# Kernel tuning notes

Hardware: AMD Instinct MI355X
Metric: run time of the kernel (lower is better)

The kernel has to match this reference:

```python
import jax, jax.numpy as jnp
import numpy as np

B, CH, H, W = 4, 256, 48, 160
A = 36            # num anchors
STRIDE = 8
KH = KW = 3       # kernel size
K2 = KH * KW
PAD = 1
THRESH = 0.5
TOPK = 3


def _offset_table():
    """Replicates shape_align.__init__ offset buffer: [1, A, 2*K2, H, W].
    Channel 2*k is the h-offset, 2*k+1 the w-offset for kernel tap k=i*KW+j."""
    rng = np.random.default_rng(0)
    ws = rng.uniform(16.0, 400.0, A).astype(np.float32)   # anchor widths (px)
    hs = rng.uniform(16.0, 300.0, A).astype(np.float32)   # anchor heights (px)
    hstep = hs / STRIDE / KH
    wstep = ws / STRIDE / KW
    off = np.zeros((1, A, 2 * K2, H, W), np.float32)
    for i in range(KH):
        for j in range(KW):
            kk = i * KW + j
            off[0, :, 2 * kk, :, :] = ((hstep - 1.0) * (i - KH / 2 + 0.5))[:, None, None]
            off[0, :, 2 * kk + 1, :, :] = ((wstep - 1.0) * (j - KW / 2 + 0.5))[:, None, None]
    return jnp.asarray(off)


def setup_inputs() -> dict:
    key = jax.random.key(0)
    k1, k2, k3 = jax.random.split(key, 3)
    x = jax.random.normal(k1, (B, CH, H, W), jnp.float32)
    prob = jax.random.uniform(k2, (B, A, H, W), jnp.float32)  # in [0,1), thresh=0.5
    weight = jax.random.normal(k3, (CH, CH, KH, KW), jnp.float32) * 0.02
    bias = jnp.zeros((CH,), jnp.float32)
    return {"x": x, "prob": prob, "offset_table": _offset_table(),
            "weight": weight, "bias": bias, "k": TOPK}


def _dcnv2(x, offset, mask, weight, bias):
    """Modulated deformable conv v2, stride=1, pad=1, dilation=1, 1 deform group.
    x: [B,C,H,W]; offset: [B,2*K2,H,W] ((h,w) interleaved); mask: [B,K2,H,W]."""
    b, c, h, w = x.shape
    off = offset.reshape(b, K2, 2, h, w)
    ki = (jnp.arange(K2) // KW - PAD).astype(x.dtype)   # kernel row offsets
    kj = (jnp.arange(K2) % KW - PAD).astype(x.dtype)    # kernel col offsets
    hg = jnp.arange(h, dtype=x.dtype)
    wg = jnp.arange(w, dtype=x.dtype)
    py = hg[None, None, :, None] + ki[None, :, None, None] + off[:, :, 0]  # [B,K2,H,W]
    px = wg[None, None, None, :] + kj[None, :, None, None] + off[:, :, 1]
    y0 = jnp.floor(py); x0 = jnp.floor(px)
    dy = py - y0; dx = px - x0
    y0i = y0.astype(jnp.int32); x0i = x0.astype(jnp.int32)
    y1i = y0i + 1;              x1i = x0i + 1
    xflat = x.reshape(b, c, h * w)

    def corner(yi, xi, wgt):
        valid = ((yi >= 0) & (yi < h) & (xi >= 0) & (xi < w)).astype(x.dtype)
        idx = (jnp.clip(yi, 0, h - 1) * w + jnp.clip(xi, 0, w - 1)).reshape(b, 1, K2 * h * w)
        g = jnp.take_along_axis(xflat, idx, axis=2)          # [B,C,K2*H*W]
        return g * (wgt * valid).reshape(b, 1, K2 * h * w)

    val = (corner(y0i, x0i, (1 - dy) * (1 - dx)) +
           corner(y0i, x1i, (1 - dy) * dx) +
           corner(y1i, x0i, dy * (1 - dx)) +
           corner(y1i, x1i, dy * dx))
    col = val.reshape(b, c, K2, h, w) * mask[:, None]        # modulation
    out = jnp.einsum('ock,bckhw->bohw', weight.reshape(weight.shape[0], c, K2), col)
    return out + bias[None, :, None, None]


def _forward(x, prob, offset_table, weight, bias, k):
    b, _, h, w = x.shape
    noff = offset_table.shape[2]                              # 2*K2
    # top-k anchor gating over anchor axis
    pk, ik = jax.lax.top_k(jnp.transpose(prob, (0, 2, 3, 1)), k)  # [B,H,W,k]
    pk = jnp.transpose(pk, (0, 3, 1, 2))                      # [B,k,H,W]
    ik = jnp.transpose(ik, (0, 3, 1, 2))
    sm = jax.nn.softmax(pk, axis=1)
    m = jnp.max(pk, axis=1, keepdims=True)                    # [B,1,H,W]
    hard = (m > THRESH).astype(x.dtype)
    # gather per-pixel offsets of the selected anchors
    tab = jnp.broadcast_to(offset_table, (b,) + offset_table.shape[1:])
    idx = jnp.broadcast_to(ik[:, :, None], (b, k, noff, h, w))
    off = jnp.take_along_axis(tab, idx, axis=1)               # [B,k,2*K2,H,W]
    off = jnp.sum(off * sm[:, :, None], axis=1) * hard        # [B,2*K2,H,W]
    mrep = jnp.repeat(m, K2, axis=1)                          # [B,K2,H,W]
    return _dcnv2(x, off, mrep, weight, bias) + x


def reference(x, prob, offset_table, weight, bias, k):
    return _forward(x, prob, offset_table, weight, bias, k)
```

## Files before the change

### kernel.cpp

```cpp
#include <hip/hip_runtime.h>
#include <math.h>

#define B_    4
#define CH_   256
#define H_    48
#define W_    160
#define A_    36
#define K2_   9
#define HW_   (H_*W_)
#define NPIX_ (B_*HW_)
#define KTOT_ (CH_*K2_)
#define CPC_  32
#define KC_   (CPC_*K2_)
#define NCHK_ (CH_/CPC_)
#define NKST_ (KTOT_/32)
#define LSTR_ 296
#define PT2_  64
#define NBLK_ (NPIX_/PT2_)

typedef __attribute__((ext_vector_type(8))) short bf16x8;
typedef __attribute__((ext_vector_type(4))) float f32x4;

__device__ inline ushort f2bf(float f) {
    union { float f; unsigned u; } c; c.f = f;
    unsigned r = c.u + 0x7FFFu + ((c.u >> 16) & 1u);
    return (ushort)(r >> 16);
}
__device__ inline float bf2f(ushort u) {
    union { unsigned u; float f; } c; c.u = (unsigned)u << 16; return c.f;
}

__global__ __launch_bounds__(256)
void prep_weight2(const float* __restrict__ w, ushort* __restrict__ wp2) {
    int t = blockIdx.x * 256 + threadIdx.x;
    if (t >= CH_ * KTOT_) return;
    int j    = t & 7;
    int lane = (t >> 3) & 63;
    int kk   = t >> 9;
    int kst  = kk % NKST_;
    int rg   = kk / NKST_;
    int row  = rg * 16 + (lane & 15);
    int kq   = kst * 32 + (lane >> 4) * 8 + j;
    int chunk = kq / KC_, r = kq % KC_;
    int tap = r / CPC_, ci = r % CPC_;
    int c = chunk * CPC_ + ci;
    wp2[t] = f2bf(w[(row * CH_ + c) * K2_ + tap]);
}

__global__ __launch_bounds__(256)
void prep_weight(const float* __restrict__ w, ushort* __restrict__ wp) {
    int t = blockIdx.x * 256 + threadIdx.x;
    if (t >= CH_ * KTOT_) return;
    int o  = t / KTOT_, kk = t % KTOT_;
    int chunk = kk / KC_, r = kk % KC_;
    int tap = r / CPC_, ci = r % CPC_;
    int c = chunk * CPC_ + ci;
    wp[t] = f2bf(w[(o * CH_ + c) * K2_ + tap]);
}

__global__ __launch_bounds__(256)
void prep_xt(const float* __restrict__ x, ushort* __restrict__ xt) {
    int bid = blockIdx.x;
    int hwT = bid % (HW_ / 128);
    int rest = bid / (HW_ / 128);
    int cT = rest & 3;
    int b  = rest >> 2;
    int hw0 = hwT * 128, c0 = cT * 64;
    int tid = threadIdx.x;
    int u = tid & 7, s = tid >> 3;
    const float* xb = x + ((long)b * CH_ + c0 + u * 8) * HW_ + hw0 + s * 4;
    float4 L[8];
    #pragma unroll
    for (int i = 0; i < 8; ++i) L[i] = *(const float4*)(xb + (long)i * HW_);
    ushort* xo = xt + ((long)b * HW_ + hw0 + s * 4) * CH_ + c0 + u * 8;
    #pragma unroll
    for (int j = 0; j < 4; ++j) {
        bf16x8 o;
        #pragma unroll
        for (int i = 0; i < 8; ++i) {
            float f = (j == 0) ? L[i].x : (j == 1) ? L[i].y : (j == 2) ? L[i].z : L[i].w;
            o[i] = (short)f2bf(f);
        }
        *(bf16x8*)(xo + (long)j * CH_) = o;
    }
}

__global__ __launch_bounds__(256)
void gating_kernel(const float* __restrict__ prob,
                   const float* __restrict__ table,
                   float* __restrict__ m_out,
                   float* __restrict__ off_out) {
    int pix = blockIdx.x * 256 + threadIdx.x;
    if (pix >= NPIX_) return;
    int b  = pix / HW_;
    int hw = pix % HW_;
    const float* pr = prob + (long)b * A_ * HW_ + hw;

    float v0 = -1e30f, v1 = -1e30f, v2 = -1e30f;
    int   i0 = 0, i1 = 0, i2 = 0;
    #pragma unroll 4
    for (int a = 0; a < A_; ++a) {
        float v = pr[(long)a * HW_];
        if (v > v0)      { v2=v1; i2=i1; v1=v0; i1=i0; v0=v; i0=a; }
        else if (v > v1) { v2=v1; i2=i1; v1=v;  i1=a; }
        else if (v > v2) { v2=v;  i2=a; }
    }
    float e1 = expf(v1 - v0), e2 = expf(v2 - v0);
    float inv = 1.0f / (1.0f + e1 + e2);
    float s0 = inv, s1 = e1*inv, s2 = e2*inv;
    float hard = (v0 > 0.5f) ? 1.0f : 0.0f;

    m_out[pix] = v0;
    const float* t0 = table + ((long)i0 * 18) * HW_ + hw;
    const float* t1 = table + ((long)i1 * 18) * HW_ + hw;
    const float* t2 = table + ((long)i2 * 18) * HW_ + hw;
    float* op = off_out + (long)pix * 18;
    #pragma unroll
    for (int c = 0; c < 18; ++c) {
        float o = s0 * t0[(long)c * HW_] + s1 * t1[(long)c * HW_] + s2 * t2[(long)c * HW_];
        op[c] = o * hard;
    }
}

__global__ __launch_bounds__(576)
void conv_mfma11(const float* __restrict__ x,
                 const ushort* __restrict__ xt,
                 const ushort* __restrict__ wp2,
                 const float* __restrict__ prob,
                 const float* __restrict__ table,
                 const float* __restrict__ bias,
                 float* __restrict__ out) {
    __shared__ __align__(16) ushort col[2][PT2_ * LSTR_];
    __shared__ float off_l[PT2_ * 18];
    __shared__ float m_l[PT2_];

    const int tid  = threadIdx.x;
    const int lane = tid & 63;
    const int wv   = tid >> 6;
    const int l15  = lane & 15;
    const int l16  = lane >> 4;
    const int bid  = (int)blockIdx.x;
    const int bswz = (bid & 7) * (NBLK_ / 8) + (bid >> 3);
    const int pb   = bswz * PT2_;
    const int b    = pb / HW_;
    const int hw0  = pb % HW_;
    const long xb  = (long)b * CH_ * HW_;
    const ushort* xtb = xt + (long)b * HW_ * CH_;

    if (tid < PT2_) {
        const int px = tid;
        const int hw = hw0 + px;
        const float* pr = prob + (long)b * A_ * HW_ + hw;
        float v0 = -1e30f, v1 = -1e30f, v2 = -1e30f;
        int   i0 = 0, i1 = 0, i2 = 0;
        #pragma unroll 4
        for (int a = 0; a < A_; ++a) {
            float v = pr[(long)a * HW_];
            if (v > v0)      { v2=v1; i2=i1; v1=v0; i1=i0; v0=v; i0=a; }
            else if (v > v1) { v2=v1; i2=i1; v1=v;  i1=a; }
            else if (v > v2) { v2=v;  i2=a; }
        }
        float e1 = expf(v1 - v0), e2 = expf(v2 - v0);
        float inv = 1.0f / (1.0f + e1 + e2);
        float s0 = inv, s1 = e1*inv, s2 = e2*inv;
        float hard = (v0 > 0.5f) ? 1.0f : 0.0f;
        m_l[px] = v0;
        const float* t0 = table + ((long)i0 * 18) * HW_ + hw;
        const float* t1 = table + ((long)i1 * 18) * HW_ + hw;
        const float* t2 = table + ((long)i2 * 18) * HW_ + hw;
        #pragma unroll
        for (int c = 0; c < 18; ++c) {
            float o = s0 * t0[(long)c * HW_] + s1 * t1[(long)c * HW_] + s2 * t2[(long)c * HW_];
            off_l[px * 18 + c] = o * hard;
        }
    }
    __syncthreads();

    const int sseg = lane & 3;
    const int qd   = lane >> 2;
    int   coff[4][4];
    float cwgt[4][4];
    int   dsto[4];
    #pragma unroll
    for (int g = 0; g < 4; ++g) {
        int pr = g * 144 + wv * 16 + qd;
        int px = pr & 63, kt = pr >> 6;
        int hw = hw0 + px;
        int h  = hw / W_, w_ = hw % W_;
        float m    = m_l[px];
        float offh = off_l[px * 18 + 2*kt];
        float offw = off_l[px * 18 + 2*kt + 1];
        float py  = (float)(h  + (kt / 3 - 1)) + offh;
        float pxf = (float)(w_ + (kt % 3 - 1)) + offw;
        float y0f = floorf(py), x0f = floorf(pxf);
        float dy = py - y0f,   dx = pxf - x0f;
        int y0 = (int)y0f, x0i = (int)x0f;
        int y1 = y0 + 1,   x1  = x0i + 1;
        float vy0 = (y0  >= 0 && y0  < H_) ? 1.f : 0.f;
        float vy1 = (y1  >= 0 && y1  < H_) ? 1.f : 0.f;
        float vx0 = (x0i >= 0 && x0i < W_) ? 1.f : 0.f;
        float vx1 = (x1  >= 0 && x1  < W_) ? 1.f : 0.f;
        int cy0 = min(max(y0, 0),  H_-1), cy1 = min(max(y1, 0), H_-1);
        int cx0 = min(max(x0i, 0), W_-1), cx1 = min(max(x1, 0), W_-1);
        coff[g][0] = (cy0*W_ + cx0) * CH_;  cwgt[g][0] = (1.f-dy)*(1.f-dx)*vy0*vx0*m;
        coff[g][1] = (cy0*W_ + cx1) * CH_;  cwgt[g][1] = (1.f-dy)*dx      *vy0*vx1*m;
        coff[g][2] = (cy1*W_ + cx0) * CH_;  cwgt[g][2] = dy      *(1.f-dx)*vy1*vx0*m;
        coff[g][3] = (cy1*W_ + cx1) * CH_;  cwgt[g][3] = dy      *dx      *vy1*vx1*m;
        dsto[g] = px * LSTR_ + kt * CPC_ + sseg * 8;
    }

    f32x4 acc[2][4];
    #pragma unroll
    for (int m = 0; m < 2; ++m)
        #pragma unroll
        for (int n = 0; n < 4; ++n)
            acc[m][n] = (f32x4)(0.f);

    const int rg0 = wv * 2;
    const int mg  = wv * 32;

    bf16x8 d[2][4];

    auto LOADpair = [&](int chI, int g0) {
        const int cb0 = chI * CPC_ + sseg * 8;
        #pragma unroll
        for (int gg = 0; gg < 2; ++gg)
            #pragma unroll
            for (int c = 0; c < 4; ++c)
                d[gg][c] = *(const bf16x8*)(xtb + coff[g0 + gg][c] + cb0);
    };
    auto WRITEpair = [&](int bufi, int g0) {
        #pragma unroll
        for (int gg = 0; gg < 2; ++gg) {
            float a8[8];
            #pragma unroll
            for (int j = 0; j < 8; ++j) a8[j] = 0.f;
            #pragma unroll
            for (int c = 0; c < 4; ++c) {
                float wgt = cwgt[g0 + gg][c];
                #pragma unroll
                for (int j = 0; j < 8; ++j)
                    a8[j] = fmaf(wgt, bf2f((ushort)d[gg][c][j]), a8[j]);
            }
            bf16x8 o;
            #pragma unroll
            for (int j = 0; j < 8; ++j) o[j] = (short)f2bf(a8[j]);
            *(bf16x8*)(&col[bufi][dsto[g0 + gg]]) = o;
        }
    };
    auto COMPUTEhalf = [&](int bufi, int chI, int ks0, int ks1) {
        if (wv < 8) {
            for (int ks = ks0; ks < ks1; ++ks) {
                const int kst = chI * K2_ + ks;
                const ushort* wr = wp2 + (((long)rg0 * NKST_ + kst) << 9) + (lane << 3);
                bf16x8 a0 = *(const bf16x8*)(wr);
                bf16x8 a1 = *(const bf16x8*)(wr + (1l * NKST_ << 9));
                const ushort* cb = &col[bufi][l15 * LSTR_ + ks * 32 + 8 * l16];
                bf16x8 b0 = *(const bf16x8*)(cb);
                bf16x8 b1 = *(const bf16x8*)(cb + 16 * LSTR_);
                bf16x8 b2 = *(const bf16x8*)(cb + 32 * LSTR_);
                bf16x8 b3 = *(const bf16x8*)(cb + 48 * LSTR_);
                __builtin_amdgcn_s_setprio(1);
                acc[0][0] = __builtin_amdgcn_mfma_f32_16x16x32_bf16(a0, b0, acc[0][0], 0, 0, 0);
                acc[0][1] = __builtin_amdgcn_mfma_f32_16x16x32_bf16(a0, b1, acc[0][1], 0, 0, 0);
                acc[0][2] = __builtin_amdgcn_mfma_f32_16x16x32_bf16(a0, b2, acc[0][2], 0, 0, 0);
                acc[0][3] = __builtin_amdgcn_mfma_f32_16x16x32_bf16(a0, b3, acc[0][3], 0, 0, 0);
                acc[1][0] = __builtin_amdgcn_mfma_f32_16x16x32_bf16(a1, b0, acc[1][0], 0, 0, 0);
                acc[1][1] = __builtin_amdgcn_mfma_f32_16x16x32_bf16(a1, b1, acc[1][1], 0, 0, 0);
                acc[1][2] = __builtin_amdgcn_mfma_f32_16x16x32_bf16(a1, b2, acc[1][2], 0, 0, 0);
                acc[1][3] = __builtin_amdgcn_mfma_f32_16x16x32_bf16(a1, b3, acc[1][3], 0, 0, 0);
                __builtin_amdgcn_s_setprio(0);
            }
        }
    };

    LOADpair(0, 0); WRITEpair(0, 0);
    LOADpair(0, 2); WRITEpair(0, 2);
    __syncthreads();

    for (int chI = 0; chI < NCHK_; ++chI) {
        const int cur = chI & 1, nxt = cur ^ 1;
        const bool pf = (chI < NCHK_ - 1);
        if (pf) LOADpair(chI + 1, 0);
        COMPUTEhalf(cur, chI, 0, 4);
        if (pf) { WRITEpair(nxt, 0); LOADpair(chI + 1, 2); }
        COMPUTEhalf(cur, chI, 4, 9);
        if (pf) WRITEpair(nxt, 2);
        __syncthreads();
    }

    if (wv < 8) {
        #pragma unroll
        for (int m = 0; m < 2; ++m)
            #pragma unroll
            for (int n = 0; n < 4; ++n)
                #pragma unroll
                for (int r = 0; r < 4; ++r) {
                    int o  = mg + m * 16 + l16 * 4 + r;
                    int hw = hw0 + n * 16 + l15;
                    long oi = xb + (long)o * HW_ + hw;
                    out[oi] = acc[m][n][r] + bias[o] + x[oi];
                }
    }
}

__global__ __launch_bounds__(576)
void conv_mfma2(const float* __restrict__ x,
                const ushort* __restrict__ wp,
                const float* __restrict__ bias,
                const float* __restrict__ m_arr,
                const float* __restrict__ off_arr,
                float* __restrict__ out) {
    __shared__ __align__(16) ushort col[PT2_ * LSTR_];

    const int tid  = threadIdx.x;
    const int lane = tid & 63;
    const int wv   = tid >> 6;
    const int l15  = lane & 15;
    const int l16  = lane >> 4;
    const int pb   = blockIdx.x * PT2_;
    const int b    = pb / HW_;
    const int hw0  = pb % HW_;
    const long xb  = (long)b * CH_ * HW_;

    int   id0, id1, id2, id3;
    float wg0, wg1, wg2, wg3;
    {
        int px = lane, kt = wv;
        int hw = hw0 + px;
        int h  = hw / W_, w_ = hw % W_;
        int pix = b * HW_ + hw;
        float m    = m_arr[pix];
        float offh = off_arr[(long)pix * 18 + 2*kt];
        float offw = off_arr[(long)pix * 18 + 2*kt + 1];
        float py = (float)(h  + (kt / 3 - 1)) + offh;
        float px_= (float)(w_ + (kt % 3 - 1)) + offw;
        float y0f = floorf(py), x0f = floorf(px_);
        float dy = py - y0f,   dx = px_ - x0f;
        int y0 = (int)y0f, x0 = (int)x0f;
        int y1 = y0 + 1,   x1 = x0 + 1;
        float vy0 = (y0 >= 0 && y0 < H_) ? 1.f : 0.f;
        float vy1 = (y1 >= 0 && y1 < H_) ? 1.f : 0.f;
        float vx0 = (x0 >= 0 && x0 < W_) ? 1.f : 0.f;
        float vx1 = (x1 >= 0 && x1 < W_) ? 1.f : 0.f;
        int cy0 = min(max(y0, 0), H_-1), cy1 = min(max(y1, 0), H_-1);
        int cx0 = min(max(x0, 0), W_-1), cx1 = min(max(x1, 0), W_-1);
        id0 = cy0*W_ + cx0;  wg0 = (1.f-dy)*(1.f-dx)*vy0*vx0*m;
        id1 = cy0*W_ + cx1;  wg1 = (1.f-dy)*dx      *vy0*vx1*m;
        id2 = cy1*W_ + cx0;  wg2 = dy      *(1.f-dx)*vy1*vx0*m;
        id3 = cy1*W_ + cx1;  wg3 = dy      *dx      *vy1*vx1*m;
    }

    f32x4 acc[4][2];
    #pragma unroll
    for (int m = 0; m < 4; ++m)
        #pragma unroll
        for (int n = 0; n < 2; ++n)
            acc[m][n] = (f32x4)(0.f);

    const int mg = (wv & 3) * 64;
    const int pg = (wv >> 2) * 32;

    for (int chI = 0; chI < NCHK_; ++chI) {
        __syncthreads();
        {
            const int c0 = chI * CPC_;
            ushort* dst = &col[lane * LSTR_ + wv * CPC_];
            #pragma unroll
            for (int c8 = 0; c8 < 4; ++c8) {
                bf16x8 pk;
                #pragma unroll
                for (int j = 0; j < 8; ++j) {
                    const float* xs = x + xb + (long)(c0 + c8*8 + j) * HW_;
                    float v = wg0 * xs[id0] + wg1 * xs[id1]
                            + wg2 * xs[id2] + wg3 * xs[id3];
                    pk[j] = (short)f2bf(v);
                }
                *(bf16x8*)(dst + c8 * 8) = pk;
            }
        }
        __syncthreads();
        if (wv < 8) {
            #pragma unroll
            for (int ks = 0; ks < K2_; ++ks) {
                const int kg = chI * KC_ + ks * 32 + 8 * l16;
                const ushort* wr = wp + (long)(mg + l15) * KTOT_ + kg;
                bf16x8 a0 = *(const bf16x8*)(wr);
                bf16x8 a1 = *(const bf16x8*)(wr + 16 * KTOT_);
                bf16x8 a2 = *(const bf16x8*)(wr + 32 * KTOT_);
                bf16x8 a3 = *(const bf16x8*)(wr + 48 * KTOT_);
                const ushort* cb = &col[(pg + l15) * LSTR_ + ks * 32 + 8 * l16];
                bf16x8 b0 = *(const bf16x8*)(cb);
                bf16x8 b1 = *(const bf16x8*)(cb + 16 * LSTR_);
                acc[0][0] = __builtin_amdgcn_mfma_f32_16x16x32_bf16(a0, b0, acc[0][0], 0, 0, 0);
                acc[0][1] = __builtin_amdgcn_mfma_f32_16x16x32_bf16(a0, b1, acc[0][1], 0, 0, 0);
                acc[1][0] = __builtin_amdgcn_mfma_f32_16x16x32_bf16(a1, b0, acc[1][0], 0, 0, 0);
                acc[1][1] = __builtin_amdgcn_mfma_f32_16x16x32_bf16(a1, b1, acc[1][1], 0, 0, 0);
                acc[2][0] = __builtin_amdgcn_mfma_f32_16x16x32_bf16(a2, b0, acc[2][0], 0, 0, 0);
                acc[2][1] = __builtin_amdgcn_mfma_f32_16x16x32_bf16(a2, b1, acc[2][1], 0, 0, 0);
                acc[3][0] = __builtin_amdgcn_mfma_f32_16x16x32_bf16(a3, b0, acc[3][0], 0, 0, 0);
                acc[3][1] = __builtin_amdgcn_mfma_f32_16x16x32_bf16(a3, b1, acc[3][1], 0, 0, 0);
            }
        }
    }

    if (wv < 8) {
        #pragma unroll
        for (int m = 0; m < 4; ++m)
            #pragma unroll
            for (int n = 0; n < 2; ++n)
                #pragma unroll
                for (int r = 0; r < 4; ++r) {
                    int o  = mg + m * 16 + l16 * 4 + r;
                    int hw = hw0 + pg + n * 16 + l15;
                    long oi = xb + (long)o * HW_ + hw;
                    out[oi] = acc[m][n][r] + bias[o] + x[oi];
                }
    }
}

extern "C" void kernel_launch(void* const* d_in, const int* in_sizes, int n_in,
                              void* d_out, int out_size, void* d_ws, size_t ws_size,
                              hipStream_t stream) {
    const float* x      = (const float*)d_in[0];
    const float* prob   = (const float*)d_in[1];
    const float* table  = (const float*)d_in[2];
    const float* weight = (const float*)d_in[3];
    const float* bias   = (const float*)d_in[4];
    float* out = (float*)d_out;

    const size_t wp_bytes  = (size_t)CH_ * KTOT_ * 2;
    const size_t m_bytes   = (size_t)NPIX_ * 4;
    const size_t off_bytes = (size_t)NPIX_ * 18 * 4;
    const size_t xt_bytes  = (size_t)NPIX_ * CH_ * 2;

    ushort* wp_ws  = (ushort*)d_ws;
    float*  m_ws   = (float*)((char*)d_ws + wp_bytes);
    float*  off_ws = (float*)((char*)d_ws + wp_bytes + m_bytes);
    ushort* xt_ws  = (ushort*)((char*)d_ws + wp_bytes + m_bytes + off_bytes);

    if (ws_size >= wp_bytes + m_bytes + off_bytes + xt_bytes) {
        prep_weight2<<<(CH_ * KTOT_ + 255) / 256, 256, 0, stream>>>(weight, wp_ws);
        prep_xt<<<(HW_ / 128) * 4 * B_, 256, 0, stream>>>(x, xt_ws);
        conv_mfma11<<<NBLK_, 576, 0, stream>>>(x, xt_ws, wp_ws, prob, table, bias, out);
    } else {
        gating_kernel<<<NPIX_ / 256, 256, 0, stream>>>(prob, table, m_ws, off_ws);
        prep_weight<<<(CH_ * KTOT_ + 255) / 256, 256, 0, stream>>>(weight, wp_ws);
        conv_mfma2<<<NPIX_ / PT2_, 576, 0, stream>>>(x, wp_ws, bias, m_ws, off_ws, out);
    }
}
```

Measured before the change: 140.3 us.

## Split deformable conv into separate im2col kernel and LDS-streamed GEMM kernel

Adds an im2col kernel that computes gating and bilinear-sampled bf16 columns into a large global workspace, then a GEMM kernel that streams those columns into LDS with direct global-to-LDS loads and double buffering. The intent is to decouple the irregular gather from the MFMA loop so each kernel runs without the other's stalls. The cost is a large round trip of the column buffer through HBM, and the path only runs if the workspace is big enough.

```diff
diff --git a/kernel.cpp b/kernel.cpp
--- a/kernel.cpp
+++ b/kernel.cpp
@@ -17,6 +17,8 @@
 #define LSTR_ 296
 #define PT2_  64
 #define NBLK_ (NPIX_/PT2_)
+#define COLB_ 36864
+#define COLW_ (COLB_/2)
 
 typedef __attribute__((ext_vector_type(8))) short bf16x8;
 typedef __attribute__((ext_vector_type(4))) float f32x4;
@@ -28,6 +30,13 @@
 }
 __device__ inline float bf2f(ushort u) {
     union { unsigned u; float f; } c; c.u = (unsigned)u << 16; return c.f;
+}
+
+__device__ inline void gld_lds16(const ushort* g, ushort* l) {
+    __builtin_amdgcn_global_load_lds(
+        (const __attribute__((address_space(1))) unsigned int*)(g),
+        (__attribute__((address_space(3))) unsigned int*)(l),
+        16, 0, 0);
 }
 
 __global__ __launch_bounds__(256)
@@ -119,6 +128,206 @@
     for (int c = 0; c < 18; ++c) {
         float o = s0 * t0[(long)c * HW_] + s1 * t1[(long)c * HW_] + s2 * t2[(long)c * HW_];
         op[c] = o * hard;
+    }
+}
+
+__global__ __launch_bounds__(576)
+void im2col_k(const ushort* __restrict__ xt,
+              const float* __restrict__ prob,
+              const float* __restrict__ table,
+              ushort* __restrict__ colg) {
+    __shared__ float off_l[PT2_ * 18];
+    __shared__ float m_l[PT2_];
+
+    const int tid  = threadIdx.x;
+    const int lane = tid & 63;
+    const int wv   = tid >> 6;
+    const int bid  = (int)blockIdx.x;
+    const int bswz = (bid & 7) * (NBLK_ / 8) + (bid >> 3);
+    const int pb   = bswz * PT2_;
+    const int b    = pb / HW_;
+    const int hw0  = pb % HW_;
+    const ushort* xtb = xt + (long)b * HW_ * CH_;
+    ushort* cg = colg + (long)bswz * (NCHK_ * COLW_);
+
+    if (tid < PT2_) {
+        const int px = tid;
+        const int hw = hw0 + px;
+        const float* pr = prob + (long)b * A_ * HW_ + hw;
+        float v0 = -1e30f, v1 = -1e30f, v2 = -1e30f;
+        int   i0 = 0, i1 = 0, i2 = 0;
+        #pragma unroll 4
+        for (int a = 0; a < A_; ++a) {
+            float v = pr[(long)a * HW_];
+            if (v > v0)      { v2=v1; i2=i1; v1=v0; i1=i0; v0=v; i0=a; }
+            else if (v > v1) { v2=v1; i2=i1; v1=v;  i1=a; }
+            else if (v > v2) { v2=v;  i2=a; }
+        }
+        float e1 = expf(v1 - v0), e2 = expf(v2 - v0);
+        float inv = 1.0f / (1.0f + e1 + e2);
+        float s0 = inv, s1 = e1*inv, s2 = e2*inv;
+        float hard = (v0 > 0.5f) ? 1.0f : 0.0f;
+        m_l[px] = v0;
+        const float* t0 = table + ((long)i0 * 18) * HW_ + hw;
+        const float* t1 = table + ((long)i1 * 18) * HW_ + hw;
+        const float* t2 = table + ((long)i2 * 18) * HW_ + hw;
+        #pragma unroll
+        for (int c = 0; c < 18; ++c) {
+            float o = s0 * t0[(long)c * HW_] + s1 * t1[(long)c * HW_] + s2 * t2[(long)c * HW_];
+            off_l[px * 18 + c] = o * hard;
+        }
+    }
+    __syncthreads();
+
+    const int sseg = lane & 3;
+    const int qd   = lane >> 2;
+    int   coff[4][4];
+    float cwgt[4][4];
+    int   gdst[4];
+    #pragma unroll
+    for (int g = 0; g < 4; ++g) {
+        int pr = g * 144 + wv * 16 + qd;
+        int px = pr & 63, kt = pr >> 6;
+        int hw = hw0 + px;
+        int h  = hw / W_, w_ = hw % W_;
+        float m    = m_l[px];
+        float offh = off_l[px * 18 + 2*kt];
+        float offw = off_l[px * 18 + 2*kt + 1];
+        float py  = (float)(h  + (kt / 3 - 1)) + offh;
+        float pxf = (float)(w_ + (kt % 3 - 1)) + offw;
+        float y0f = floorf(py), x0f = floorf(pxf);
+        float dy = py - y0f,   dx = pxf - x0f;
+        int y0 = (int)y0f, x0i = (int)x0f;
+        int y1 = y0 + 1,   x1  = x0i + 1;
+        float vy0 = (y0  >= 0 && y0  < H_) ? 1.f : 0.f;
+        float vy1 = (y1  >= 0 && y1  < H_) ? 1.f : 0.f;
+        float vx0 = (x0i >= 0 && x0i < W_) ? 1.f : 0.f;
+        float vx1 = (x1  >= 0 && x1  < W_) ? 1.f : 0.f;
+        int cy0 = min(max(y0, 0),  H_-1), cy1 = min(max(y1, 0), H_-1);
+        int cx0 = min(max(x0i, 0), W_-1), cx1 = min(max(x1, 0), W_-1);
+        coff[g][0] = (cy0*W_ + cx0) * CH_;  cwgt[g][0] = (1.f-dy)*(1.f-dx)*vy0*vx0*m;
+        coff[g][1] = (cy0*W_ + cx1) * CH_;  cwgt[g][1] = (1.f-dy)*dx      *vy0*vx1*m;
+        coff[g][2] = (cy1*W_ + cx0) * CH_;  cwgt[g][2] = dy      *(1.f-dx)*vy1*vx0*m;
+        coff[g][3] = (cy1*W_ + cx1) * CH_;  cwgt[g][3] = dy      *dx      *vy1*vx1*m;
+        gdst[g] = ((kt * 4 + sseg) * 64 + px) * 8;
+    }
+
+    for (int chI = 0; chI < NCHK_; ++chI) {
+        const int cb0 = chI * CPC_ + sseg * 8;
+        bf16x8 d[4][4];
+        #pragma unroll
+        for (int g = 0; g < 4; ++g)
+            #pragma unroll
+            for (int c = 0; c < 4; ++c)
+                d[g][c] = *(const bf16x8*)(xtb + coff[g][c] + cb0);
+        ushort* cgo = cg + (long)chI * COLW_;
+        #pragma unroll
+        for (int g = 0; g < 4; ++g) {
+            float a8[8];
+            #pragma unroll
+            for (int j = 0; j < 8; ++j) a8[j] = 0.f;
+            #pragma unroll
+            for (int c = 0; c < 4; ++c) {
+                float wgt = cwgt[g][c];
+                #pragma unroll
+                for (int j = 0; j < 8; ++j)
+                    a8[j] = fmaf(wgt, bf2f((ushort)d[g][c][j]), a8[j]);
+            }
+            bf16x8 o;
+            #pragma unroll
+            for (int j = 0; j < 8; ++j) o[j] = (short)f2bf(a8[j]);
+            *(bf16x8*)(cgo + gdst[g]) = o;
+        }
+    }
+}
+
+__global__ __launch_bounds__(576)
+void conv_gemm(const float* __restrict__ x,
+               const ushort* __restrict__ colg,
+               const ushort* __restrict__ wp2,
+               const float* __restrict__ bias,
+               float* __restrict__ out) {
+    __shared__ __align__(16) ushort colL[2][COLW_];
+
+    const int tid  = threadIdx.x;
+    const int lane = tid & 63;
+    const int wv   = tid >> 6;
+    const int l15  = lane & 15;
+    const int l16  = lane >> 4;
+    const int bid  = (int)blockIdx.x;
+    const int bswz = (bid & 7) * (NBLK_ / 8) + (bid >> 3);
+    const int pb   = bswz * PT2_;
+    const int b    = pb / HW_;
+    const int hw0  = pb % HW_;
+    const long xb  = (long)b * CH_ * HW_;
+    const ushort* cg = colg + (long)bswz * (NCHK_ * COLW_);
+
+    f32x4 acc[2][4];
+    #pragma unroll
+    for (int m = 0; m < 2; ++m)
+        #pragma unroll
+        for (int n = 0; n < 4; ++n)
+            acc[m][n] = (f32x4)(0.f);
+
+    const int rg0 = wv * 2;
+    const int mg  = wv * 32;
+
+    auto STAGE = [&](int chI, int bufi) {
+        const ushort* src = cg + (long)chI * COLW_;
+        #pragma unroll
+        for (int i = 0; i < 4; ++i) {
+            const int go = (wv * 4 + i) * 512;
+            gld_lds16(src + go + lane * 8, (ushort*)colL[bufi] + go);
+        }
+    };
+    auto COMPUTE = [&](int bufi, int chI) {
+        if (wv < 8) {
+            #pragma unroll
+            for (int ks = 0; ks < K2_; ++ks) {
+                const int kst = chI * K2_ + ks;
+                const ushort* wr = wp2 + (((long)rg0 * NKST_ + kst) << 9) + (lane << 3);
+                bf16x8 a0 = *(const bf16x8*)(wr);
+                bf16x8 a1 = *(const bf16x8*)(wr + (1l * NKST_ << 9));
+                const ushort* cb = &colL[bufi][((ks * 4 + l16) * 64 + l15) * 8];
+                bf16x8 b0 = *(const bf16x8*)(cb);
+                bf16x8 b1 = *(const bf16x8*)(cb + 16 * 8);
+                bf16x8 b2 = *(const bf16x8*)(cb + 32 * 8);
+                bf16x8 b3 = *(const bf16x8*)(cb + 48 * 8);
+                __builtin_amdgcn_s_setprio(1);
+                acc[0][0] = __builtin_amdgcn_mfma_f32_16x16x32_bf16(a0, b0, acc[0][0], 0, 0, 0);
+                acc[0][1] = __builtin_amdgcn_mfma_f32_16x16x32_bf16(a0, b1, acc[0][1], 0, 0, 0);
+                acc[0][2] = __builtin_amdgcn_mfma_f32_16x16x32_bf16(a0, b2, acc[0][2], 0, 0, 0);
+                acc[0][3] = __builtin_amdgcn_mfma_f32_16x16x32_bf16(a0, b3, acc[0][3], 0, 0, 0);
+                acc[1][0] = __builtin_amdgcn_mfma_f32_16x16x32_bf16(a1, b0, acc[1][0], 0, 0, 0);
+                acc[1][1] = __builtin_amdgcn_mfma_f32_16x16x32_bf16(a1, b1, acc[1][1], 0, 0, 0);
+                acc[1][2] = __builtin_amdgcn_mfma_f32_16x16x32_bf16(a1, b2, acc[1][2], 0, 0, 0);
+                acc[1][3] = __builtin_amdgcn_mfma_f32_16x16x32_bf16(a1, b3, acc[1][3], 0, 0, 0);
+                __builtin_amdgcn_s_setprio(0);
+            }
+        }
+    };
+
+    STAGE(0, 0);
+    __syncthreads();
+    for (int chI = 0; chI < NCHK_; ++chI) {
+        const int cur = chI & 1, nxt = cur ^ 1;
+        if (chI < NCHK_ - 1) STAGE(chI + 1, nxt);
+        COMPUTE(cur, chI);
+        __syncthreads();
+    }
+
+    if (wv < 8) {
+        #pragma unroll
+        for (int m = 0; m < 2; ++m)
+            #pragma unroll
+            for (int n = 0; n < 4; ++n)
+                #pragma unroll
+                for (int r = 0; r < 4; ++r) {
+                    int o  = mg + m * 16 + l16 * 4 + r;
+                    int hw = hw0 + n * 16 + l15;
+                    long oi = xb + (long)o * HW_ + hw;
+                    out[oi] = acc[m][n][r] + bias[o] + x[oi];
+                }
     }
 }
 
@@ -433,13 +642,23 @@
     const size_t m_bytes   = (size_t)NPIX_ * 4;
     const size_t off_bytes = (size_t)NPIX_ * 18 * 4;
     const size_t xt_bytes  = (size_t)NPIX_ * CH_ * 2;
+    const size_t col_bytes = (size_t)NBLK_ * NCHK_ * COLB_;
 
     ushort* wp_ws  = (ushort*)d_ws;
     float*  m_ws   = (float*)((char*)d_ws + wp_bytes);
     float*  off_ws = (float*)((char*)d_ws + wp_bytes + m_bytes);
     ushort* xt_ws  = (ushort*)((char*)d_ws + wp_bytes + m_bytes + off_bytes);
-
-    if (ws_size >= wp_bytes + m_bytes + off_bytes + xt_bytes) {
+    ushort* col_ws = (ushort*)((char*)d_ws + wp_bytes + m_bytes + off_bytes + xt_bytes);
+
+    const size_t need_v11 = wp_bytes + m_bytes + off_bytes + xt_bytes;
+    const size_t need_v13 = need_v11 + col_bytes;
+
+    if (ws_size >= need_v13) {
+        prep_weight2<<<(CH_ * KTOT_ + 255) / 256, 256, 0, stream>>>(weight, wp_ws);
+        prep_xt<<<(HW_ / 128) * 4 * B_, 256, 0, stream>>>(x, xt_ws);
+        im2col_k<<<NBLK_, 576, 0, stream>>>(xt_ws, prob, table, col_ws);
+        conv_gemm<<<NBLK_, 576, 0, stream>>>(x, col_ws, wp_ws, bias, out);
+    } else if (ws_size >= need_v11) {
         prep_weight2<<<(CH_ * KTOT_ + 255) / 256, 256, 0, stream>>>(weight, wp_ws);
         prep_xt<<<(HW_ / 128) * 4 * B_, 256, 0, stream>>>(x, xt_ws);
         conv_mfma11<<<NBLK_, 576, 0, stream>>>(x, xt_ws, wp_ws, prob, table, bias, out);
```

After: 174.9 us. 24.7% more time.
